# Performance work log

Measured on AMD Instinct MI355X. Metric: run time of the kernel, lower is better.

## Reference

```python
import jax, jax.numpy as jnp
import numpy as np

B, S, D = 4, 2048, 1024


def setup_inputs() -> dict:
    key = jax.random.key(0)
    k1, k2 = jax.random.split(key)
    x = jax.random.normal(k1, (B, S, D), dtype=jnp.float32)
    W_qkv = jax.random.normal(k2, (D, 3 * D), dtype=jnp.float32) * 0.02
    # causal mask: 1 where attendable, 0 where masked (broadcast over batch)
    attention_mask = jnp.tril(jnp.ones((S, S), dtype=jnp.int32))[None, :, :]
    return {"input": x, "W_qkv": W_qkv, "attention_mask": attention_mask}


def reference(input, W_qkv, attention_mask):
    # fused QKV projection (nn.Linear, bias=False)
    qkv = jnp.einsum('bsd,de->bse', input, W_qkv)  # [B, S, 3D]
    q, k, v = jnp.split(qkv, 3, axis=-1)           # each [B, S, D]
    scale = 1.0 / jnp.sqrt(jnp.asarray(D, dtype=input.dtype))
    scores = jnp.einsum('bqd,bkd->bqk', q, k) * scale  # [B, S, S]
    neg_inf = jnp.finfo(scores.dtype).min
    scores = jnp.where(attention_mask == 0, neg_inf, scores)
    attn = jax.nn.softmax(scores, axis=-1)
    # dropout prob = 0.0 -> identity
    out = jnp.einsum('bqk,bkd->bqd', attn, v)      # [B, S, D]
    return out
```

## Files before the change

### kernel.cpp

```cpp
#include <hip/hip_runtime.h>
#include <hip/hip_bf16.h>


typedef __attribute__((ext_vector_type(8))) short short8;
typedef __attribute__((ext_vector_type(4))) short s16x4;
typedef __attribute__((ext_vector_type(4))) float f32x4;

__device__ __forceinline__ short f2bf(float f) {
  __hip_bfloat16 h = __float2bfloat16(f);
  return *reinterpret_cast<short*>(&h);
}

__device__ __forceinline__ void gll16(const void* g, void* l) {
  __builtin_amdgcn_global_load_lds((const __attribute__((address_space(1))) void*)g,
                                   (__attribute__((address_space(3))) void*)l,
                                   16, 0, 0);
}

__device__ __forceinline__ void gemm_core(const short* __restrict__ A,
                                          const short* __restrict__ Bt,
                                          int lda, int ldb,
                                          int row0, int col0, int kIters,
                                          f32x4 acc[4][4],
                                          short* lA, short* lB) {
  const int tid  = threadIdx.x;
  const int wave = tid >> 6;
  const int lane = tid & 63;
  const int quad = lane >> 4;
  const int l16  = lane & 15;

  const f32x4 zero = {0.f, 0.f, 0.f, 0.f};
#pragma unroll
  for (int i = 0; i < 4; ++i)
#pragma unroll
    for (int j = 0; j < 4; ++j) acc[i][j] = zero;

  const int srow = tid >> 3;
  const int gcol = ((tid & 7) ^ (srow & 7)) * 8;
  const short* A1 = A + (size_t)(row0 + srow) * lda + gcol;
  const short* A2 = A + (size_t)(row0 + srow + 32) * lda + gcol;
  const short* A3 = A + (size_t)(row0 + srow + 64) * lda + gcol;
  const short* A4 = A + (size_t)(row0 + srow + 96) * lda + gcol;
  const short* B1 = Bt + (size_t)(col0 + srow) * ldb + gcol;
  const short* B2 = Bt + (size_t)(col0 + srow + 32) * ldb + gcol;
  const short* B3 = Bt + (size_t)(col0 + srow + 64) * ldb + gcol;
  const short* B4 = Bt + (size_t)(col0 + srow + 96) * ldb + gcol;

  short* lA1 = lA + wave * 512;
  short* lA2 = lA + 2048 + wave * 512;
  short* lA3 = lA + 4096 + wave * 512;
  short* lA4 = lA + 6144 + wave * 512;
  short* lB1 = lB + wave * 512;
  short* lB2 = lB + 2048 + wave * 512;
  short* lB3 = lB + 4096 + wave * 512;
  short* lB4 = lB + 6144 + wave * 512;

  const int rswz  = l16 & 7;
  const int slot0 = (quad ^ rswz) * 8;
  const int slot1 = ((4 + quad) ^ rswz) * 8;
  const short* aRow = lA + ((wave >> 1) * 64 + l16) * 64;
  const short* bRow = lB + ((wave & 1) * 64 + l16) * 64;

  for (int it = 0; it < kIters; ++it) {
    const int k0 = it * 64;
    gll16(A1 + k0, lA1);
    gll16(A2 + k0, lA2);
    gll16(A3 + k0, lA3);
    gll16(A4 + k0, lA4);
    gll16(B1 + k0, lB1);
    gll16(B2 + k0, lB2);
    gll16(B3 + k0, lB3);
    gll16(B4 + k0, lB4);
    __syncthreads();

#pragma unroll
    for (int s = 0; s < 2; ++s) {
      const int so = s ? slot1 : slot0;
      short8 af[4], bfr[4];
#pragma unroll
      for (int i = 0; i < 4; ++i) af[i] = *(const short8*)(aRow + i * 1024 + so);
#pragma unroll
      for (int j = 0; j < 4; ++j) bfr[j] = *(const short8*)(bRow + j * 1024 + so);
#pragma unroll
      for (int i = 0; i < 4; ++i)
#pragma unroll
        for (int j = 0; j < 4; ++j)
          acc[i][j] = __builtin_amdgcn_mfma_f32_16x16x32_bf16(af[i], bfr[j], acc[i][j], 0, 0, 0);
    }
    __syncthreads();
  }
}

#define EPILOGUE_VARS                         \
  const int lane = threadIdx.x & 63;          \
  const int wave = threadIdx.x >> 6;          \
  const int quad = lane >> 4;                 \
  const int l16  = lane & 15;                 \
  const int rb   = (wave >> 1) * 64;          \
  const int cb   = (wave & 1) * 64;

__global__ __launch_bounds__(256) void setup_kernel(const float* __restrict__ X,
                                                    const float* __restrict__ W,
                                                    short* __restrict__ Xb,
                                                    short* __restrict__ Wt,
                                                    float* __restrict__ rs) {
  const int bid = blockIdx.x;
  if (bid < 8192) {
    const int i = (bid * 256 + threadIdx.x) * 4;
    const f32x4 v = *(const f32x4*)(X + i);
    s16x4 o;
    o.x = f2bf(v.x); o.y = f2bf(v.y); o.z = f2bf(v.z); o.w = f2bf(v.w);
    *(s16x4*)(Xb + i) = o;
  } else if (bid < 11264) {
    __shared__ float tile[32][33];
    const int r  = bid - 8192;
    const int ni = r % 96;
    const int ki = r / 96;
    const int tx = threadIdx.x & 31;
    const int ty = threadIdx.x >> 5;
#pragma unroll
    for (int rr = 0; rr < 4; ++rr)
      tile[ty + rr * 8][tx] = W[(size_t)(ki * 32 + ty + rr * 8) * 3072 + ni * 32 + tx];
    __syncthreads();
#pragma unroll
    for (int rr = 0; rr < 4; ++rr)
      Wt[(size_t)(ni * 32 + ty + rr * 8) * 1024 + ki * 32 + tx] = f2bf(tile[tx][ty + rr * 8]);
  } else {
    const int i = (bid - 11264) * 1024 + threadIdx.x * 4;
    const f32x4 zero = {0.f, 0.f, 0.f, 0.f};
    *(f32x4*)(rs + i) = zero;
  }
}

__global__ __launch_bounds__(256) void qkv_gemm_kernel(const short* __restrict__ Xb,
                                                       const short* __restrict__ Wt,
                                                       short* __restrict__ Q,
                                                       short* __restrict__ K,
                                                       short* __restrict__ Vt,
                                                       int br0) {
  __shared__ short lA[8192], lB[8192];
  const int br = br0 + blockIdx.x / 24;
  const int bc = blockIdx.x % 24;
  f32x4 acc[4][4];
  gemm_core(Xb, Wt, 1024, 1024, br * 128, bc * 128, 16, acc, lA, lB);

  EPILOGUE_VARS
  const int rbase = br * 128 + rb;
  const int cbase = bc * 128 + cb;
  if (bc < 16) {
#pragma unroll
    for (int i = 0; i < 4; ++i)
#pragma unroll
      for (int j = 0; j < 4; ++j) {
        const int col = cbase + j * 16 + l16;
        short* dst = (col < 1024) ? Q : K;
        const int n = col & 1023;
#pragma unroll
        for (int r = 0; r < 4; ++r) {
          const int row = rbase + i * 16 + quad * 4 + r;
          dst[(size_t)row * 1024 + n] = f2bf(acc[i][j][r]);
        }
      }
  } else {
    const int b  = rbase >> 11;
    const int s0 = rbase & 2047;
    short* VtB = Vt + (size_t)b * 1024 * 2048;
#pragma unroll
    for (int i = 0; i < 4; ++i) {
      const int sb = s0 + i * 16 + quad * 4;
#pragma unroll
      for (int j = 0; j < 4; ++j) {
        const int d = cbase - 2048 + j * 16 + l16;
        s16x4 pk;
        pk.x = f2bf(acc[i][j][0]);
        pk.y = f2bf(acc[i][j][1]);
        pk.z = f2bf(acc[i][j][2]);
        pk.w = f2bf(acc[i][j][3]);
        *(s16x4*)(VtB + (size_t)d * 2048 + sb) = pk;
      }
    }
  }
}

__global__ __launch_bounds__(256) void qk_kernel(const short* __restrict__ Q,
                                                 const short* __restrict__ K,
                                                 short* __restrict__ E,
                                                 float* __restrict__ rs) {
  __shared__ short lA[8192], lB[8192];
  const int orig = blockIdx.x;
  const int t = (orig & 7) * 68 + (orig >> 3);
  const int b = t / 136;
  int off = t % 136;
  int qi = 15;
  while (off >= qi + 1) { off -= qi + 1; qi--; }
  const int ki = off;

  f32x4 acc[4][4];
  const short* Qb = Q + (size_t)b * 2048 * 1024;
  const short* Kb = K + (size_t)b * 2048 * 1024;
  gemm_core(Qb, Kb, 1024, 1024, qi * 128, ki * 128, 16, acc, lA, lB);

  EPILOGUE_VARS
  short* Eb  = E + (size_t)b * 2048 * 2048;
  float* rsb = rs + b * 2048;
  const int rbase = qi * 128 + rb;
  const int cbase = ki * 128 + cb;
  const bool diag = (ki == qi);
#pragma unroll
  for (int i = 0; i < 4; ++i)
#pragma unroll
    for (int r = 0; r < 4; ++r) {
      const int row = rbase + i * 16 + quad * 4 + r;
      float partial = 0.f;
#pragma unroll
      for (int j = 0; j < 4; ++j) {
        const int col = cbase + j * 16 + l16;
        float e = __expf(acc[i][j][r] * 0.03125f);
        if (diag && col > row) e = 0.f;
        partial += e;
        Eb[(size_t)row * 2048 + col] = f2bf(e);
      }
      partial += __shfl_xor(partial, 1);
      partial += __shfl_xor(partial, 2);
      partial += __shfl_xor(partial, 4);
      partial += __shfl_xor(partial, 8);
      if (l16 == 0) atomicAdd(rsb + row, partial);
    }
}

__global__ __launch_bounds__(256) void pv_kernel(const short* __restrict__ E,
                                                 const short* __restrict__ Vt,
                                                 const float* __restrict__ rs,
                                                 float* __restrict__ out) {
  __shared__ short lA[8192], lB[8192];
  const int t   = blockIdx.x;
  const int b   = t >> 7;
  const int rem = t & 127;
  const int qi  = 15 - (rem >> 3);
  const int dj  = rem & 7;

  f32x4 acc[4][4];
  const short* Eb  = E + (size_t)b * 2048 * 2048;
  const short* Vtb = Vt + (size_t)b * 1024 * 2048;
  gemm_core(Eb, Vtb, 2048, 2048, qi * 128, dj * 128, (qi + 1) * 2, acc, lA, lB);

  EPILOGUE_VARS
  float* ob = out + (size_t)b * 2048 * 1024;
  const float* rsb = rs + b * 2048;
  const int rbase = qi * 128 + rb;
  const int cbase = dj * 128 + cb;
#pragma unroll
  for (int i = 0; i < 4; ++i)
#pragma unroll
    for (int r2 = 0; r2 < 4; ++r2) {
      const int row = rbase + i * 16 + quad * 4 + r2;
      const float inv = 1.f / rsb[row];
#pragma unroll
      for (int j = 0; j < 4; ++j) {
        const int col = cbase + j * 16 + l16;
        ob[(size_t)row * 1024 + col] = acc[i][j][r2] * inv;
      }
    }
}

extern "C" void kernel_launch(void* const* d_in, const int* in_sizes, int n_in,
                              void* d_out, int out_size, void* d_ws, size_t ws_size,
                              hipStream_t stream) {
  const float* X = (const float*)d_in[0];
  const float* W = (const float*)d_in[1];
  float* out = (float*)d_out;
  char* w = (char*)d_ws;

  short* Xb = (short*)(w + 0);
  short* Wt = (short*)(w + 16777216);
  short* E  = (short*)(w + 0);
  float* rs = (float*)(w + 50331648);
  short* Q  = (short*)(w + 67108864);
  short* K  = (short*)(w + 83886080);
  short* Vt = (short*)(w + 100663296);

  hipLaunchKernelGGL(setup_kernel,    dim3(11272), dim3(256), 0, stream, X, W, Xb, Wt, rs);
  hipLaunchKernelGGL(qkv_gemm_kernel, dim3(768),   dim3(256), 0, stream, Xb, Wt, Q, K, Vt, 0);
  hipLaunchKernelGGL(qkv_gemm_kernel, dim3(768),   dim3(256), 0, stream, Xb, Wt, Q, K, Vt, 32);
  hipLaunchKernelGGL(qk_kernel,       dim3(544),   dim3(256), 0, stream, Q, K, E, rs);
  hipLaunchKernelGGL(pv_kernel,       dim3(512),   dim3(256), 0, stream, E, Vt, rs, out);
}
```

Baseline: 247.0 us.

## Add triple-buffered direct-to-LDS GEMM core for attention GEMMs and nontemporal stores

Adds a new GEMM core that uses a three-stage LDS ring with K-step 32, issuing global_load_lds prefetches three iterations ahead and waiting on explicit vmcnt counts, so memory latency overlaps MFMA work. The QK and PV kernels now use this core, and the QK block-to-tile mapping is changed to interleave batches instead of using the old swizzle. All intermediate and output stores become nontemporal to cut cache pollution. The cost is more LDS per block, which may lower occupancy, and twice as many barrier-synchronised iterations.

```diff
diff --git a/kernel.cpp b/kernel.cpp
--- a/kernel.cpp
+++ b/kernel.cpp
@@ -16,6 +16,10 @@
                                    (__attribute__((address_space(3))) void*)l,
                                    16, 0, 0);
 }
+
+__device__ __forceinline__ void ntst_s(short* p, short v)   { __builtin_nontemporal_store(v, p); }
+__device__ __forceinline__ void ntst_s4(s16x4* p, s16x4 v)  { __builtin_nontemporal_store(v, p); }
+__device__ __forceinline__ void ntst_f(float* p, float v)   { __builtin_nontemporal_store(v, p); }
 
 __device__ __forceinline__ void gemm_core(const short* __restrict__ A,
                                           const short* __restrict__ Bt,
@@ -91,6 +95,82 @@
   }
 }
 
+__device__ __forceinline__ void gemm_core_p3(const short* __restrict__ A,
+                                             const short* __restrict__ Bt,
+                                             int lda, int ldb,
+                                             int row0, int col0, int kIters,
+                                             f32x4 acc[4][4], short* lds) {
+  const int tid  = threadIdx.x;
+  const int wave = tid >> 6;
+  const int lane = tid & 63;
+  const int quad = lane >> 4;
+  const int l16  = lane & 15;
+
+  const f32x4 zero = {0.f, 0.f, 0.f, 0.f};
+#pragma unroll
+  for (int i = 0; i < 4; ++i)
+#pragma unroll
+    for (int j = 0; j < 4; ++j) acc[i][j] = zero;
+
+  const int srow = tid >> 2;
+  const int gcol = ((tid & 3) ^ (srow & 3)) * 8;
+  const short* Ag = A  + (size_t)(row0 + srow) * lda + gcol;
+  const short* Bg = Bt + (size_t)(col0 + srow) * ldb + gcol;
+  const size_t a64 = (size_t)64 * lda;
+  const size_t b64 = (size_t)64 * ldb;
+
+  const int rb = (wave >> 1) * 64;
+  const int cb = (wave & 1) * 64;
+  const int slot = (quad ^ (l16 & 3)) * 8;
+  const int aoff = (rb + l16) * 32 + slot;
+  const int boff = 4096 + (cb + l16) * 32 + slot;
+
+#define P3_ISSUE(sl, itv) do {                        \
+    short* st_ = lds + (sl) * 8192 + wave * 512;      \
+    const int k0_ = (itv) * 32;                       \
+    gll16(Ag + k0_,        st_);                      \
+    gll16(Ag + a64 + k0_,  st_ + 2048);               \
+    gll16(Bg + k0_,        st_ + 4096);               \
+    gll16(Bg + b64 + k0_,  st_ + 6144);               \
+  } while (0)
+
+  P3_ISSUE(0, 0);
+  P3_ISSUE(1, 1);
+  P3_ISSUE(2, 2);
+
+  int s = 0;
+  for (int it = 0; it < kIters; ++it) {
+    if (it < kIters - 2)       asm volatile("s_waitcnt vmcnt(8)" ::: "memory");
+    else if (it == kIters - 2) asm volatile("s_waitcnt vmcnt(4)" ::: "memory");
+    else                       asm volatile("s_waitcnt vmcnt(0)" ::: "memory");
+    __builtin_amdgcn_sched_barrier(0);
+    __builtin_amdgcn_s_barrier();
+
+    const short* st = lds + s * 8192;
+    short8 af[4], bfr[4];
+#pragma unroll
+    for (int i = 0; i < 4; ++i) af[i]  = *(const short8*)(st + aoff + i * 512);
+#pragma unroll
+    for (int j = 0; j < 4; ++j) bfr[j] = *(const short8*)(st + boff + j * 512);
+
+    asm volatile("s_waitcnt lgkmcnt(0)" ::: "memory");
+    __builtin_amdgcn_sched_barrier(0);
+    __builtin_amdgcn_s_barrier();
+
+    if (it + 3 < kIters) P3_ISSUE(s, it + 3);
+    __builtin_amdgcn_sched_barrier(0);
+
+#pragma unroll
+    for (int i = 0; i < 4; ++i)
+#pragma unroll
+      for (int j = 0; j < 4; ++j)
+        acc[i][j] = __builtin_amdgcn_mfma_f32_16x16x32_bf16(af[i], bfr[j], acc[i][j], 0, 0, 0);
+
+    s = (s == 2) ? 0 : s + 1;
+  }
+#undef P3_ISSUE
+}
+
 #define EPILOGUE_VARS                         \
   const int lane = threadIdx.x & 63;          \
   const int wave = threadIdx.x >> 6;          \
@@ -110,7 +190,7 @@
     const f32x4 v = *(const f32x4*)(X + i);
     s16x4 o;
     o.x = f2bf(v.x); o.y = f2bf(v.y); o.z = f2bf(v.z); o.w = f2bf(v.w);
-    *(s16x4*)(Xb + i) = o;
+    ntst_s4((s16x4*)(Xb + i), o);
   } else if (bid < 11264) {
     __shared__ float tile[32][33];
     const int r  = bid - 8192;
@@ -124,7 +204,8 @@
     __syncthreads();
 #pragma unroll
     for (int rr = 0; rr < 4; ++rr)
-      Wt[(size_t)(ni * 32 + ty + rr * 8) * 1024 + ki * 32 + tx] = f2bf(tile[tx][ty + rr * 8]);
+      ntst_s(&Wt[(size_t)(ni * 32 + ty + rr * 8) * 1024 + ki * 32 + tx],
+             f2bf(tile[tx][ty + rr * 8]));
   } else {
     const int i = (bid - 11264) * 1024 + threadIdx.x * 4;
     const f32x4 zero = {0.f, 0.f, 0.f, 0.f};
@@ -158,7 +239,7 @@
 #pragma unroll
         for (int r = 0; r < 4; ++r) {
           const int row = rbase + i * 16 + quad * 4 + r;
-          dst[(size_t)row * 1024 + n] = f2bf(acc[i][j][r]);
+          ntst_s(&dst[(size_t)row * 1024 + n], f2bf(acc[i][j][r]));
         }
       }
   } else {
@@ -176,7 +257,7 @@
         pk.y = f2bf(acc[i][j][1]);
         pk.z = f2bf(acc[i][j][2]);
         pk.w = f2bf(acc[i][j][3]);
-        *(s16x4*)(VtB + (size_t)d * 2048 + sb) = pk;
+        ntst_s4((s16x4*)(VtB + (size_t)d * 2048 + sb), pk);
       }
     }
   }
@@ -186,19 +267,17 @@
                                                  const short* __restrict__ K,
                                                  short* __restrict__ E,
                                                  float* __restrict__ rs) {
-  __shared__ short lA[8192], lB[8192];
-  const int orig = blockIdx.x;
-  const int t = (orig & 7) * 68 + (orig >> 3);
-  const int b = t / 136;
-  int off = t % 136;
-  int qi = 15;
+  __shared__ short lds[24576];
+  const int t = blockIdx.x >> 2;
+  const int b = blockIdx.x & 3;
+  int qi = 15, off = t;
   while (off >= qi + 1) { off -= qi + 1; qi--; }
   const int ki = off;
 
   f32x4 acc[4][4];
   const short* Qb = Q + (size_t)b * 2048 * 1024;
   const short* Kb = K + (size_t)b * 2048 * 1024;
-  gemm_core(Qb, Kb, 1024, 1024, qi * 128, ki * 128, 16, acc, lA, lB);
+  gemm_core_p3(Qb, Kb, 1024, 1024, qi * 128, ki * 128, 32, acc, lds);
 
   EPILOGUE_VARS
   short* Eb  = E + (size_t)b * 2048 * 2048;
@@ -218,7 +297,7 @@
         float e = __expf(acc[i][j][r] * 0.03125f);
         if (diag && col > row) e = 0.f;
         partial += e;
-        Eb[(size_t)row * 2048 + col] = f2bf(e);
+        ntst_s(&Eb[(size_t)row * 2048 + col], f2bf(e));
       }
       partial += __shfl_xor(partial, 1);
       partial += __shfl_xor(partial, 2);
@@ -232,7 +311,7 @@
                                                  const short* __restrict__ Vt,
                                                  const float* __restrict__ rs,
                                                  float* __restrict__ out) {
-  __shared__ short lA[8192], lB[8192];
+  __shared__ short lds[24576];
   const int t   = blockIdx.x;
   const int b   = t >> 7;
   const int rem = t & 127;
@@ -242,7 +321,7 @@
   f32x4 acc[4][4];
   const short* Eb  = E + (size_t)b * 2048 * 2048;
   const short* Vtb = Vt + (size_t)b * 1024 * 2048;
-  gemm_core(Eb, Vtb, 2048, 2048, qi * 128, dj * 128, (qi + 1) * 2, acc, lA, lB);
+  gemm_core_p3(Eb, Vtb, 2048, 2048, qi * 128, dj * 128, (qi + 1) * 4, acc, lds);
 
   EPILOGUE_VARS
   float* ob = out + (size_t)b * 2048 * 1024;
@@ -258,7 +337,7 @@
 #pragma unroll
       for (int j = 0; j < 4; ++j) {
         const int col = cbase + j * 16 + l16;
-        ob[(size_t)row * 1024 + col] = acc[i][j][r2] * inv;
+        ntst_f(&ob[(size_t)row * 1024 + col], acc[i][j][r2] * inv);
       }
     }
 }
```

Result: slower. 270.2 us (+9.4%).
